# Kernel tuning notes

Hardware: AMD Instinct MI355X
Metric: run time of the kernel (lower is better)

Reference implementation:

```python
import jax, jax.numpy as jnp
import numpy as np

H, N_PATCH, F, DIM = 12, 196, 8, 768
DH = DIM // H            # 64
D3 = 3 * DH              # per-head dim after 3*dim projection = 192
SCALE = float(np.sqrt(DH) * H)
B, S = 8, 1 + N_PATCH * F  # 1569


def setup_inputs() -> dict:
    key = jax.random.key(0)
    ks = jax.random.split(key, 12)
    w = lambda k, shp: (jax.random.normal(k, shp, dtype=jnp.float32) * 0.02)
    return {
        "x": jax.random.normal(ks[0], (B, S, DIM), dtype=jnp.float32),
        "Wq": w(ks[1], (DIM, 3 * DIM)), "bq": jnp.zeros((3 * DIM,), jnp.float32),
        "Wk": w(ks[2], (DIM, 3 * DIM)), "bk": jnp.zeros((3 * DIM,), jnp.float32),
        "Wv": w(ks[3], (DIM, 3 * DIM)), "bv": jnp.zeros((3 * DIM,), jnp.float32),
        "Wt": w(ks[4], (3 * DIM, DIM)), "bt": jnp.zeros((DIM,), jnp.float32),
        "Wf": w(ks[5], (3 * DIM, DIM)), "bf": jnp.zeros((DIM,), jnp.float32),
    }


def _heads(t):
    # [b, s, 3*dim] -> [b, H, s, D3]
    b, s, _ = t.shape
    return t.reshape(b, s, H, D3).transpose(0, 2, 1, 3)


def _merge(t):
    # [b, H, s, D3] -> [b, s, 3*dim]
    b, _, s, _ = t.shape
    return t.transpose(0, 2, 1, 3).reshape(b, s, H * D3)


def _attn(q, k, v):
    a = jax.nn.softmax(jnp.einsum('bhqd,bhkd->bhqk', q, k) / SCALE, axis=-1)
    return jnp.einsum('bhqk,bhkd->bhqd', a, v)


def reference(x, Wq, bq, Wk, bk, Wv, bv, Wt, bt, Wf, bf):
    patches = x[:, 1:, :]                       # [b, n*F, dim]
    # NOTE: faithful to original code: v_mat comes from self.k, k_mat from self.v
    qm = _heads(patches @ Wq + bq)
    vm = _heads(patches @ Wk + bk)
    km = _heads(patches @ Wv + bv)

    # CLS attention over full sequence (here v from self.v, k from self.k)
    q_cls = _heads(x[:, 0:1, :] @ Wq + bq)      # [b,H,1,D3]
    v_cls = _heads(x @ Wv + bv)
    k_cls = _heads(x @ Wk + bk)
    inter_cls = _attn(q_cls, k_cls, v_cls)      # [b,H,1,D3]

    # Stage 1: temporal attention per patch (patches 1..n-1), vectorized.
    # tokens are frame-major: index = frame*n + patch, so slice p::n == patch p across frames
    def per_patch(t):
        b = t.shape[0]
        return t.reshape(b, H, F, N_PATCH, D3)[:, :, :, 1:, :].transpose(0, 1, 3, 2, 4)  # [b,H,n-1,F,D3]
    q5, k5, v5 = per_patch(qm), per_patch(km), per_patch(vm)
    a1 = jax.nn.softmax(jnp.einsum('bhpfd,bhpgd->bhpfg', q5, k5) / SCALE, axis=-1)
    t1 = jnp.einsum('bhpfg,bhpgd->bhpfd', a1, v5).sum(axis=3)   # [b,H,n-1,D3]
    t1 = jnp.tile(t1, (1, 1, F, 1))                              # [b,H,(n-1)*F,D3]
    ti = _merge(t1) @ Wt + bt                                    # [b,(n-1)*F,dim]

    # Stage 2 (same qkv swap as stage 1)
    q2 = _heads(ti @ Wq + bq)
    v2 = _heads(ti @ Wk + bk)
    k2 = _heads(ti @ Wv + bv)
    outs = [_attn(q2[:, :, 0:N_PATCH], k2[:, :, 0:N_PATCH], v2[:, :, 0:N_PATCH]).sum(axis=2, keepdims=True)]
    for xi in range(1, F):  # small fixed loop over num_frames
        o = _attn(q2[:, :, xi:xi + N_PATCH], k2[:, :, xi::N_PATCH], v2[:, :, xi::N_PATCH])
        outs.append(o.sum(axis=2, keepdims=True))
    t2 = jnp.concatenate(outs, axis=2)                           # [b,H,F,D3]
    t2 = jnp.tile(t2, (1, 1, N_PATCH, 1))                        # [b,H,F*n,D3]

    full = jnp.concatenate([inter_cls, t2], axis=2)              # [b,H,1+n*F,D3]
    return _merge(full) @ Wf + bf                                # [b,S,dim]
```

## Files before the change

### kernel.cpp

```cpp
#include <hip/hip_runtime.h>
#include <math.h>

#define B_    8
#define SEQ   1569
#define DIMX  768
#define H_    12
#define D3    192
#define F_    8
#define NP    196
#define P1    195
#define NCOL  2304
#define NS    6912
#define RSCALE (1.0f/96.0f)
#define NCHUNK 16
#define CH     99
#define CLS_STRIDE 196
#define PG4   49

typedef __bf16 bf16_t;
typedef bf16_t bf16x8 __attribute__((ext_vector_type(8)));
typedef float  f32x4  __attribute__((ext_vector_type(4)));

__device__ __forceinline__ void load_lds16(const bf16_t* g, bf16_t* l) {
  __builtin_amdgcn_global_load_lds(
      (const __attribute__((address_space(1))) void*)g,
      (__attribute__((address_space(3))) void*)l, 16, 0, 0);
}

__device__ __forceinline__ float block_max256(float v, float* red) {
  #pragma unroll
  for (int o = 32; o > 0; o >>= 1) v = fmaxf(v, __shfl_xor(v, o, 64));
  __syncthreads();
  if ((threadIdx.x & 63) == 0) red[threadIdx.x >> 6] = v;
  __syncthreads();
  return fmaxf(fmaxf(red[0], red[1]), fmaxf(red[2], red[3]));
}

__device__ __forceinline__ float block_sum256(float v, float* red) {
  #pragma unroll
  for (int o = 32; o > 0; o >>= 1) v += __shfl_xor(v, o, 64);
  __syncthreads();
  if ((threadIdx.x & 63) == 0) red[threadIdx.x >> 6] = v;
  __syncthreads();
  return red[0] + red[1] + red[2] + red[3];
}

__global__ __launch_bounds__(256) void cast_f32_bf16(
    const float* __restrict__ in, bf16_t* __restrict__ out, int n4) {
  const int i = blockIdx.x * 256 + threadIdx.x;
  if (i >= n4) return;
  const float4 v = ((const float4*)in)[i];
  bf16_t o4[4] = {(bf16_t)v.x, (bf16_t)v.y, (bf16_t)v.z, (bf16_t)v.w};
  ((uint2*)out)[i] = *(uint2*)o4;
}

__global__ __launch_bounds__(256) void concat_bias_kernel(
    const float* __restrict__ bq, const float* __restrict__ bk,
    const float* __restrict__ bv, float* __restrict__ qkvb) {
  const int i = blockIdx.x * 256 + threadIdx.x;
  if (i >= NS) return;
  float v;
  if (i < NCOL) v = bq[i];
  else if (i < 2 * NCOL) v = bk[i - NCOL];
  else v = bv[i - 2 * NCOL];
  qkvb[i] = v;
}

__global__ __launch_bounds__(256) void transpose_all(
    const float* __restrict__ Wq, const float* __restrict__ Wk,
    const float* __restrict__ Wv, const float* __restrict__ Wt,
    const float* __restrict__ Wf, bf16_t* __restrict__ WqkvT,
    bf16_t* __restrict__ WtT, bf16_t* __restrict__ WfT) {
  __shared__ float t[32][33];
  const int bid = blockIdx.x;
  const int mat = bid / 1728, tt = bid % 1728;
  const float* W; bf16_t* WT; int Kd, Nd, nt, kt;
  if (mat < 3) {
    Kd = DIMX; Nd = NCOL;
    W = (mat == 0) ? Wq : ((mat == 1) ? Wk : Wv);
    WT = WqkvT + (size_t)mat * NCOL * DIMX;
    nt = tt % 72; kt = tt / 72;
  } else {
    Kd = NCOL; Nd = DIMX;
    W = (mat == 3) ? Wt : Wf;
    WT = (mat == 3) ? WtT : WfT;
    nt = tt % 24; kt = tt / 24;
  }
  const int bn = nt * 32, bk = kt * 32;
  const int tx = threadIdx.x & 31, ty = threadIdx.x >> 5;
  #pragma unroll
  for (int i = 0; i < 32; i += 8)
    t[ty + i][tx] = W[(size_t)(bk + ty + i) * Nd + bn + tx];
  __syncthreads();
  #pragma unroll
  for (int i = 0; i < 32; i += 8)
    WT[(size_t)(bn + ty + i) * Kd + bk + tx] = (bf16_t)t[tx][ty + i];
}

__global__ __launch_bounds__(256) void gemm_mfma_bt(
    const bf16_t* __restrict__ A, const bf16_t* __restrict__ BT,
    const float* __restrict__ bias, void* __restrict__ C,
    int M, int N, int K, int MT, int NT, int GROUPM, int XCDB, int outBf16) {
  __shared__ bf16_t As[128 * 64];
  __shared__ bf16_t Bs[128 * 64];
  const int tid  = threadIdx.x;
  const int wave = tid >> 6, lane = tid & 63;

  int m_tile, n_tile;
  const int pid = blockIdx.x;
  if (XCDB > 0) {
    const int xcd = pid & 7, q = pid >> 3;
    m_tile = xcd * XCDB + q % XCDB;
    n_tile = q / XCDB;
    if (m_tile >= MT) return;
  } else {
    const int npg   = GROUPM * NT;
    const int group = pid / npg;
    const int first_m = group * GROUPM;
    int gsm = MT - first_m; if (gsm > GROUPM) gsm = GROUPM;
    const int lpid  = pid % npg;
    m_tile = first_m + lpid % gsm;
    n_tile = lpid / gsm;
  }
  const int row0 = m_tile * 128, col0 = n_tile * 128;

  const int fr = lane & 15, kg = lane >> 4;
  int ra0 = row0 + wave * 32 + fr;
  int ra1 = ra0 + 16;
  if (ra0 >= M) ra0 = M - 1;
  if (ra1 >= M) ra1 = M - 1;
  const bf16_t* Ap0 = A + (size_t)ra0 * K + kg * 8;
  const bf16_t* Ap1 = A + (size_t)ra1 * K + kg * 8;
  const bf16_t* Bp0 = BT + (size_t)(col0 + wave * 32 + fr) * K + kg * 8;
  const bf16_t* Bp1 = Bp0 + (size_t)16 * K;
  const int la0 = (wave * 2 + 0) * 1024, la1 = (wave * 2 + 1) * 1024;

  const int mb = (wave & 1) * 4,  nb = (wave >> 1) * 4;
  const int m0 = (wave & 1) * 64, n0 = (wave >> 1) * 64;
  f32x4 acc[4][4] = {};

  for (int k0 = 0; k0 < K; k0 += 64) {
    load_lds16(Ap0 + k0,      &As[la0]);
    load_lds16(Ap0 + k0 + 32, &As[la0 + 512]);
    load_lds16(Ap1 + k0,      &As[la1]);
    load_lds16(Ap1 + k0 + 32, &As[la1 + 512]);
    load_lds16(Bp0 + k0,      &Bs[la0]);
    load_lds16(Bp0 + k0 + 32, &Bs[la0 + 512]);
    load_lds16(Bp1 + k0,      &Bs[la1]);
    load_lds16(Bp1 + k0 + 32, &Bs[la1 + 512]);
    __syncthreads();

    #pragma unroll
    for (int h = 0; h < 2; ++h) {
      bf16x8 af[4], bfr[4];
      #pragma unroll
      for (int i = 0; i < 4; ++i) {
        af[i]  = *(const bf16x8*)&As[(mb + i) * 1024 + h * 512 + lane * 8];
        bfr[i] = *(const bf16x8*)&Bs[(nb + i) * 1024 + h * 512 + lane * 8];
      }
      #pragma unroll
      for (int i = 0; i < 4; ++i)
        #pragma unroll
        for (int j = 0; j < 4; ++j)
          acc[i][j] = __builtin_amdgcn_mfma_f32_16x16x32_bf16(
              af[i], bfr[j], acc[i][j], 0, 0, 0);
    }
    __syncthreads();
  }

  const int cc = lane & 15, cr4 = (lane >> 4) * 4;
  #pragma unroll
  for (int i = 0; i < 4; ++i) {
    #pragma unroll
    for (int j = 0; j < 4; ++j) {
      const int col = col0 + n0 + j * 16 + cc;
      const float bcol = bias[col];
      #pragma unroll
      for (int reg = 0; reg < 4; ++reg) {
        const int r = row0 + m0 + i * 16 + cr4 + reg;
        if (r < M) {
          const float v = acc[i][j][reg] + bcol;
          if (outBf16) ((bf16_t*)C)[(size_t)r * N + col] = (bf16_t)v;
          else         ((float*)C)[(size_t)r * N + col] = v;
        }
      }
    }
  }
}

__global__ __launch_bounds__(256) void xi0_scores_mfma(
    const bf16_t* __restrict__ QKV2, float* __restrict__ Smat) {
  __shared__ bf16_t As[128 * 32];
  __shared__ bf16_t Bs[128 * 32];
  const int tid  = threadIdx.x;
  const int wave = tid >> 6, lane = tid & 63;
  const int row0 = blockIdx.x * 128, col0 = blockIdx.y * 128;
  const int bh = blockIdx.z;
  const int b = bh / H_, h = bh % H_;
  const bf16_t* Abase = QKV2 + (size_t)b * P1 * NS + h * D3;
  const bf16_t* Bbase = QKV2 + (size_t)b * P1 * NS + 2 * NCOL + h * D3;

  const int fr = lane & 15, kg = lane >> 4;
  int ra0 = row0 + wave * 32 + fr;
  int ra1 = ra0 + 16;
  if (ra0 >= P1) ra0 = P1 - 1;
  if (ra1 >= P1) ra1 = P1 - 1;
  int cb0 = col0 + wave * 32 + fr;
  int cb1 = cb0 + 16;
  if (cb0 >= P1) cb0 = P1 - 1;
  if (cb1 >= P1) cb1 = P1 - 1;
  const bf16_t* Ap0 = Abase + (size_t)ra0 * NS + kg * 8;
  const bf16_t* Ap1 = Abase + (size_t)ra1 * NS + kg * 8;
  const bf16_t* Bp0 = Bbase + (size_t)cb0 * NS + kg * 8;
  const bf16_t* Bp1 = Bbase + (size_t)cb1 * NS + kg * 8;
  bf16_t* lA0 = &As[(wave * 2 + 0) * 512];
  bf16_t* lA1 = &As[(wave * 2 + 1) * 512];
  bf16_t* lB0 = &Bs[(wave * 2 + 0) * 512];
  bf16_t* lB1 = &Bs[(wave * 2 + 1) * 512];

  const int m0 = (wave & 1) * 64, n0 = (wave >> 1) * 64;
  const int mb = (wave & 1) * 4,  nb = (wave >> 1) * 4;
  f32x4 acc[4][4] = {};

  for (int k0 = 0; k0 < D3; k0 += 32) {
    load_lds16(Ap0 + k0, lA0);
    load_lds16(Ap1 + k0, lA1);
    load_lds16(Bp0 + k0, lB0);
    load_lds16(Bp1 + k0, lB1);
    __syncthreads();
    bf16x8 af[4], bfr[4];
    #pragma unroll
    for (int i = 0; i < 4; ++i) {
      af[i]  = *(const bf16x8*)&As[(mb + i) * 512 + lane * 8];
      bfr[i] = *(const bf16x8*)&Bs[(nb + i) * 512 + lane * 8];
    }
    #pragma unroll
    for (int i = 0; i < 4; ++i)
      #pragma unroll
      for (int j = 0; j < 4; ++j)
        acc[i][j] = __builtin_amdgcn_mfma_f32_16x16x32_bf16(
            af[i], bfr[j], acc[i][j], 0, 0, 0);
    __syncthreads();
  }

  float* S = Smat + (size_t)bh * P1 * P1;
  const int cc = lane & 15, cr4 = (lane >> 4) * 4;
  #pragma unroll
  for (int i = 0; i < 4; ++i)
    #pragma unroll
    for (int j = 0; j < 4; ++j) {
      const int col = col0 + n0 + j * 16 + cc;
      #pragma unroll
      for (int reg = 0; reg < 4; ++reg) {
        const int r = row0 + m0 + i * 16 + cr4 + reg;
        if (r < P1 && col < P1) S[(size_t)r * P1 + col] = acc[i][j][reg] * RSCALE;
      }
    }
}

__global__ __launch_bounds__(256) void xi0_finish_kernel(
    const float* __restrict__ Smat, const bf16_t* __restrict__ QKV2,
    bf16_t* __restrict__ FULL9b) {
  const int bh = blockIdx.x;
  const int b = bh / H_, h = bh % H_;
  __shared__ float mrow[P1], inv_l[P1], g[P1];
  const float* S = Smat + (size_t)bh * P1 * P1;
  const int tid = threadIdx.x;
  const int wave = tid >> 6, lane = tid & 63;

  for (int r = wave; r < P1; r += 4) {
    const float* Sr = S + (size_t)r * P1;
    const float s0 = Sr[lane];
    const float s1 = Sr[64 + lane];
    const float s2 = Sr[128 + lane];
    const float s3 = (lane < 3) ? Sr[192 + lane] : -1e30f;
    float m = fmaxf(fmaxf(s0, s1), fmaxf(s2, s3));
    #pragma unroll
    for (int o = 1; o < 64; o <<= 1) m = fmaxf(m, __shfl_xor(m, o, 64));
    float e = expf(s0 - m) * ((lane == 0) ? 2.f : 1.f) + expf(s1 - m) +
              expf(s2 - m) + ((lane < 3) ? expf(s3 - m) : 0.f);
    #pragma unroll
    for (int o = 1; o < 64; o <<= 1) e += __shfl_xor(e, o, 64);
    if (lane == 0) {
      mrow[r] = m;
      inv_l[r] = ((r == 0) ? 2.f : 1.f) / e;
    }
  }
  __syncthreads();
  if (tid < P1) {
    float s = 0.f;
    for (int r = 0; r < P1; ++r)
      s += expf(S[(size_t)r * P1 + tid] - mrow[r]) * inv_l[r];
    g[tid] = s * ((tid == 0) ? 2.f : 1.f);
  }
  __syncthreads();
  if (tid < D3) {
    float acc = 0.f;
    const bf16_t* vbase = QKV2 + (size_t)b * P1 * NS + NCOL + h * D3 + tid;
    for (int k = 0; k < P1; ++k)
      acc = fmaf(g[k], (float)vbase[(size_t)k * NS], acc);
    FULL9b[((size_t)b * 9 + 1) * NCOL + h * D3 + tid] = (bf16_t)acc;
  }
}

__global__ __launch_bounds__(256) void cls_part_kernel(
    const bf16_t* __restrict__ XQKV, float* __restrict__ CLSP, int b0) {
  const int h  = blockIdx.x % H_;
  const int bl = blockIdx.x / H_;
  const int b  = b0 + bl;
  const int c  = blockIdx.y;
  const int t0 = c * CH;
  const int tend = (t0 + CH < SEQ) ? t0 + CH : SEQ;
  __shared__ float qs[D3];
  __shared__ float sc[CH];
  __shared__ float red[4];
  const int tid = threadIdx.x;

  const bf16_t* Qr = XQKV + (size_t)bl * SEQ * NS + h * D3;
  if (tid < 24) {
    const bf16x8 q8 = *(const bf16x8*)(Qr + tid * 8);
    #pragma unroll
    for (int m2 = 0; m2 < 8; ++m2) qs[tid * 8 + m2] = (float)q8[m2];
  }
  __syncthreads();

  float lmax = -1e30f;
  for (int t = t0 + tid; t < tend; t += 256) {
    const bf16_t* kr = XQKV + ((size_t)bl * SEQ + t) * NS + NCOL + h * D3;
    float acc = 0.f;
    #pragma unroll 3
    for (int d = 0; d < D3; d += 8) {
      const bf16x8 k8 = *(const bf16x8*)(kr + d);
      #pragma unroll
      for (int m2 = 0; m2 < 8; ++m2) acc = fmaf(qs[d + m2], (float)k8[m2], acc);
    }
    acc *= RSCALE;
    sc[t - t0] = acc;
    lmax = fmaxf(lmax, acc);
  }
  const float m = block_max256(lmax, red);
  float lsum = 0.f;
  for (int t = t0 + tid; t < tend; t += 256) {
    const float e = expf(sc[t - t0] - m);
    sc[t - t0] = e;
    lsum += e;
  }
  const float L = block_sum256(lsum, red);
  __syncthreads();

  float* P = CLSP + ((size_t)(b * H_ + h) * NCHUNK + c) * CLS_STRIDE;
  if (tid < D3) {
    float acc = 0.f;
    const bf16_t* vbase = XQKV + ((size_t)bl * SEQ + t0) * NS + 2 * NCOL + h * D3 + tid;
    for (int t = t0; t < tend; ++t)
      acc = fmaf(sc[t - t0], (float)vbase[(size_t)(t - t0) * NS], acc);
    P[tid] = acc;
  }
  if (tid == 192) P[192] = m;
  if (tid == 193) P[193] = L;
}

__global__ __launch_bounds__(256) void cls_combine_kernel(
    const float* __restrict__ CLSP, bf16_t* __restrict__ FULL9b) {
  const int bh = blockIdx.x;
  const int tid = threadIdx.x;
  const float* P = CLSP + (size_t)bh * NCHUNK * CLS_STRIDE;

  float M = -1e30f;
  #pragma unroll
  for (int c = 0; c < NCHUNK; ++c) M = fmaxf(M, P[c * CLS_STRIDE + 192]);
  float L = 0.f;
  float w[NCHUNK];
  #pragma unroll
  for (int c = 0; c < NCHUNK; ++c) {
    w[c] = expf(P[c * CLS_STRIDE + 192] - M);
    L += P[c * CLS_STRIDE + 193] * w[c];
  }
  if (tid < D3) {
    float acc = 0.f;
    #pragma unroll
    for (int c = 0; c < NCHUNK; ++c)
      acc = fmaf(w[c], P[c * CLS_STRIDE + tid], acc);
    const int b = bh / H_, h = bh % H_;
    FULL9b[((size_t)b * 9 + 0) * NCOL + h * D3 + tid] = (bf16_t)(acc / L);
  }
}

__global__ __launch_bounds__(256) void temporal_kernel(
    const bf16_t* __restrict__ XQKV, bf16_t* __restrict__ T1U, int b0) {
  const int id = blockIdx.x;
  const int pg = id % PG4;
  const int h  = (id / PG4) % H_;
  const int bl = id / (PG4 * H_);
  const int b  = b0 + bl;
  const int wave = threadIdx.x >> 6, lane = threadIdx.x & 63;
  __shared__ float qs[4][8][196], ks[4][8][196];

  int pi = pg * 4 + wave;
  const bool act = (pi < P1);
  if (!act) pi = P1 - 1;

  #pragma unroll
  for (int i = 0; i < 6; ++i) {
    const int idx = lane + 64 * i;
    const int arr = idx / 192;
    const int c = idx % 192;
    const int f = c / 24, d0 = (c % 24) * 8;
    const size_t base = ((size_t)bl * SEQ + (size_t)f * NP + pi + 2) * NS +
                        (arr ? 2 * NCOL : 0) + h * D3 + d0;
    const bf16x8 v8 = *(const bf16x8*)(XQKV + base);
    float* dst = arr ? &ks[wave][f][d0] : &qs[wave][f][d0];
    #pragma unroll
    for (int m2 = 0; m2 < 8; ++m2) dst[m2] = (float)v8[m2];
  }
  __syncthreads();

  const int f = lane >> 3, g = lane & 7;
  float s = 0.f;
  for (int d = 0; d < D3; d += 4) {
    const float4 a4 = *(const float4*)&qs[wave][f][d];
    const float4 b4 = *(const float4*)&ks[wave][g][d];
    s = fmaf(a4.x, b4.x, s); s = fmaf(a4.y, b4.y, s);
    s = fmaf(a4.z, b4.z, s); s = fmaf(a4.w, b4.w, s);
  }
  s *= RSCALE;

  float m = s;
  #pragma unroll
  for (int o = 1; o < 8; o <<= 1) m = fmaxf(m, __shfl_xor(m, o, 64));
  const float e = expf(s - m);
  float sum = e;
  #pragma unroll
  for (int o = 1; o < 8; o <<= 1) sum += __shfl_xor(sum, o, 64);
  float a = e / sum;
  #pragma unroll
  for (int o = 8; o < 64; o <<= 1) a += __shfl_xor(a, o, 64);
  float wg[8];
  #pragma unroll
  for (int gg = 0; gg < 8; ++gg) wg[gg] = __shfl(a, gg, 64);

  if (act) {
    const size_t vrow = (size_t)bl * SEQ * NS + NCOL + h * D3;
    #pragma unroll
    for (int i = 0; i < 3; ++i) {
      const int d = lane + 64 * i;
      float o = 0.f;
      #pragma unroll
      for (int gg = 0; gg < 8; ++gg) {
        const bf16_t vv = XQKV[vrow + ((size_t)gg * NP + pi + 2) * NS + d];
        o = fmaf(wg[gg], (float)vv, o);
      }
      T1U[((size_t)b * P1 + pi) * NCOL + h * D3 + d] = (bf16_t)o;
    }
  }
}

__global__ __launch_bounds__(256) void stage2_xi_kernel(
    const bf16_t* __restrict__ QKV2, bf16_t* __restrict__ FULL9b) {
  const int xi = 1 + blockIdx.x % 7;
  const int h  = (blockIdx.x / 7) % H_;
  const int b  = blockIdx.x / (7 * H_);
  __shared__ float Ks[8][196], Vs[8][196], Qs[32][196];
  __shared__ float Pp[32][8];
  const int tid = threadIdx.x;

  for (int idx = tid; idx < 192; idx += 256) {
    const int k = idx / 24, d0 = (idx % 24) * 8;
    const bf16x8 v8 = *(const bf16x8*)(QKV2 + ((size_t)(b * P1 + xi + k)) * NS +
                                       2 * NCOL + h * D3 + d0);
    #pragma unroll
    for (int m2 = 0; m2 < 8; ++m2) Ks[k][d0 + m2] = (float)v8[m2];
  }
  for (int idx = tid; idx < 192; idx += 256) {
    const int k = idx / 24, d0 = (idx % 24) * 8;
    const bf16x8 v8 = *(const bf16x8*)(QKV2 + ((size_t)(b * P1 + xi + k)) * NS +
                                       NCOL + h * D3 + d0);
    #pragma unroll
    for (int m2 = 0; m2 < 8; ++m2) Vs[k][d0 + m2] = (float)v8[m2];
  }

  float acc = 0.f;
  for (int c = 0; c < 7; ++c) {
    __syncthreads();
    for (int idx = tid; idx < 768; idx += 256) {
      const int qr = idx / 24, d0 = (idx % 24) * 8;
      const int rq = c * 32 + qr;
      if (rq < P1) {
        const bf16x8 v8 = *(const bf16x8*)(QKV2 + ((size_t)(b * P1 + rq)) * NS +
                                           h * D3 + d0);
        #pragma unroll
        for (int m2 = 0; m2 < 8; ++m2) Qs[qr][d0 + m2] = (float)v8[m2];
      } else {
        #pragma unroll
        for (int m2 = 0; m2 < 8; ++m2) Qs[qr][d0 + m2] = 0.f;
      }
    }
    __syncthreads();
    const int grp = tid >> 3, k = tid & 7;
    float dot = 0.f;
    for (int d = 0; d < D3; d += 4) {
      const float4 a4 = *(const float4*)&Qs[grp][d];
      const float4 b4 = *(const float4*)&Ks[k][d];
      dot = fmaf(a4.x, b4.x, dot); dot = fmaf(a4.y, b4.y, dot);
      dot = fmaf(a4.z, b4.z, dot); dot = fmaf(a4.w, b4.w, dot);
    }
    dot *= RSCALE;
    float m = dot;
    #pragma unroll
    for (int o = 1; o < 8; o <<= 1) m = fmaxf(m, __shfl_xor(m, o, 64));
    const float e = expf(dot - m);
    float s = e;
    #pragma unroll
    for (int o = 1; o < 8; o <<= 1) s += __shfl_xor(s, o, 64);
    Pp[grp][k] = e / s;
    __syncthreads();
    if (tid < D3) {
      #pragma unroll 4
      for (int g2 = 0; g2 < 32; ++g2) {
        const int rq2 = c * 32 + g2;
        if (rq2 < P1) {
          const float mult = (rq2 == xi) ? 2.f : 1.f;
          float o = 0.f;
          #pragma unroll
          for (int kk = 0; kk < 8; ++kk) o = fmaf(Pp[g2][kk], Vs[kk][tid], o);
          acc = fmaf(mult, o, acc);
        }
      }
    }
  }
  if (tid < D3)
    FULL9b[((size_t)b * 9 + 1 + xi) * NCOL + h * D3 + tid] = (bf16_t)acc;
}

__global__ __launch_bounds__(256) void bcast_kernel(
    const float* __restrict__ OUT9, float* __restrict__ out) {
  const int idx = blockIdx.x * 256 + threadIdx.x;
  const int total = B_ * SEQ * (DIMX / 4);
  if (idx >= total) return;
  const int d4 = idx % (DIMX / 4);
  const int bs = idx / (DIMX / 4);
  const int s = bs % SEQ;
  const int b = bs / SEQ;
  const int row = (s == 0) ? 0 : 1 + ((s - 1) & 7);
  ((float4*)out)[idx] = ((const float4*)OUT9)[(size_t)(b * 9 + row) * (DIMX / 4) + d4];
}

extern "C" void kernel_launch(void* const* d_in, const int* in_sizes, int n_in,
                              void* d_out, int out_size, void* d_ws, size_t ws_size,
                              hipStream_t stream) {
  const float* x  = (const float*)d_in[0];
  const float* Wq = (const float*)d_in[1];
  const float* bq = (const float*)d_in[2];
  const float* Wk = (const float*)d_in[3];
  const float* bk = (const float*)d_in[4];
  const float* Wv = (const float*)d_in[5];
  const float* bv = (const float*)d_in[6];
  const float* Wt = (const float*)d_in[7];
  const float* bt = (const float*)d_in[8];
  const float* Wf = (const float*)d_in[9];
  const float* bf = (const float*)d_in[10];
  float* out = (float*)d_out;
  (void)in_sizes; (void)n_in; (void)out_size;

  char* ws = (char*)d_ws;
  size_t off = 0;
  auto alloc_f32 = [&](size_t elems) {
    size_t a = (off + 63) & ~(size_t)63;
    off = a + elems * sizeof(float);
    return (float*)(ws + a);
  };
  auto alloc_bf16 = [&](size_t elems) {
    size_t a = (off + 63) & ~(size_t)63;
    off = a + elems * sizeof(bf16_t);
    return (bf16_t*)(ws + a);
  };

  bf16_t* T1Ub   = alloc_bf16((size_t)B_ * P1 * NCOL);
  bf16_t* TIUb   = alloc_bf16((size_t)B_ * P1 * DIMX);
  bf16_t* QKV2b  = alloc_bf16((size_t)B_ * P1 * NS);
  bf16_t* FULL9b = alloc_bf16((size_t)B_ * 9 * NCOL);
  float*  OUT9   = alloc_f32((size_t)B_ * 9 * DIMX);
  float*  Smat   = alloc_f32((size_t)B_ * H_ * P1 * P1);
  float*  CLSP   = alloc_f32((size_t)B_ * H_ * NCHUNK * CLS_STRIDE);
  float*  QKVbias= alloc_f32(NS);
  bf16_t* WqkvT  = alloc_bf16((size_t)3 * NCOL * DIMX);
  bf16_t* WtT    = alloc_bf16((size_t)DIMX * NCOL);
  bf16_t* WfT    = alloc_bf16((size_t)DIMX * NCOL);

  const size_t remain = (ws_size > off) ? (ws_size - off) : 0;
  int Bc = 8;
  while (Bc > 1 &&
         (size_t)Bc * SEQ * (NS + DIMX) * sizeof(bf16_t) + 512 > remain)
    Bc >>= 1;
  bf16_t* XQKVb = alloc_bf16((size_t)Bc * SEQ * NS);
  bf16_t* xb    = alloc_bf16((size_t)Bc * SEQ * DIMX);

  transpose_all<<<dim3(1728 * 5), 256, 0, stream>>>(
      Wq, Wk, Wv, Wt, Wf, WqkvT, WtT, WfT);
  concat_bias_kernel<<<dim3((NS + 255) / 256), 256, 0, stream>>>(bq, bk, bv, QKVbias);

  for (int b0 = 0; b0 < B_; b0 += Bc) {
    const int Mrows = Bc * SEQ;
    const int n4 = Mrows * DIMX / 4;
    cast_f32_bf16<<<dim3((n4 + 255) / 256), 256, 0, stream>>>(
        x + (size_t)b0 * SEQ * DIMX, xb, n4);
    const int MT = (Mrows + 127) / 128, NT = NS / 128;
    const int XCDB = (MT + 7) / 8;
    gemm_mfma_bt<<<dim3(8 * XCDB * NT), 256, 0, stream>>>(
        xb, WqkvT, QKVbias, XQKVb, Mrows, NS, DIMX, MT, NT, 0, XCDB, 1);
    cls_part_kernel<<<dim3(Bc * H_, NCHUNK), 256, 0, stream>>>(XQKVb, CLSP, b0);
    temporal_kernel<<<dim3(Bc * H_ * PG4), 256, 0, stream>>>(XQKVb, T1Ub, b0);
  }
  cls_combine_kernel<<<dim3(B_ * H_), 256, 0, stream>>>(CLSP, FULL9b);

  {
    const int MT = (B_ * P1 + 127) / 128, NT = DIMX / 128;
    gemm_mfma_bt<<<dim3(MT * NT), 256, 0, stream>>>(
        T1Ub, WtT, bt, TIUb, B_ * P1, DIMX, NCOL, MT, NT, 4, 0, 1);
  }
  {
    const int MT = (B_ * P1 + 127) / 128, NT = NS / 128;
    gemm_mfma_bt<<<dim3(MT * NT), 256, 0, stream>>>(
        TIUb, WqkvT, QKVbias, QKV2b, B_ * P1, NS, DIMX, MT, NT, 4, 0, 1);
  }

  xi0_scores_mfma<<<dim3(2, 2, B_ * H_), 256, 0, stream>>>(QKV2b, Smat);
  xi0_finish_kernel<<<dim3(B_ * H_), 256, 0, stream>>>(Smat, QKV2b, FULL9b);
  stage2_xi_kernel<<<dim3(B_ * H_ * 7), 256, 0, stream>>>(QKV2b, FULL9b);

  {
    const int MT = 1, NT = DIMX / 128;
    gemm_mfma_bt<<<dim3(MT * NT), 256, 0, stream>>>(
        FULL9b, WfT, bf, OUT9, B_ * 9, DIMX, NCOL, MT, NT, 1, 0, 0);
  }

  {
    const int total4 = B_ * SEQ * (DIMX / 4);
    bcast_kernel<<<dim3((total4 + 255) / 256), 256, 0, stream>>>(OUT9, out);
  }
}
```

Baseline: 816.4 us.

## Pre-swizzle weights and input into MFMA fragment panels for contiguous LDS loads

Transposed weights and the bf16-cast input are now written in a tiled panel layout of 16 rows by 32 k per 512-element block, matching the MFMA fragment order. The GEMM then loads each wave's LDS tile from one contiguous 1KB span instead of strided rows. This targets global-load coalescing in the QKV projection and the other weight-side loads. It also drops the XCD-aware tile mapping in favour of grouped-M ordering and pads the input buffer to a multiple of 128 rows.

```diff
diff --git a/kernel.cpp b/kernel.cpp
--- a/kernel.cpp
+++ b/kernel.cpp
@@ -45,15 +45,6 @@
   return red[0] + red[1] + red[2] + red[3];
 }
 
-__global__ __launch_bounds__(256) void cast_f32_bf16(
-    const float* __restrict__ in, bf16_t* __restrict__ out, int n4) {
-  const int i = blockIdx.x * 256 + threadIdx.x;
-  if (i >= n4) return;
-  const float4 v = ((const float4*)in)[i];
-  bf16_t o4[4] = {(bf16_t)v.x, (bf16_t)v.y, (bf16_t)v.z, (bf16_t)v.w};
-  ((uint2*)out)[i] = *(uint2*)o4;
-}
-
 __global__ __launch_bounds__(256) void concat_bias_kernel(
     const float* __restrict__ bq, const float* __restrict__ bk,
     const float* __restrict__ bv, float* __restrict__ qkvb) {
@@ -64,6 +55,25 @@
   else if (i < 2 * NCOL) v = bk[i - NCOL];
   else v = bv[i - 2 * NCOL];
   qkvb[i] = v;
+}
+
+__global__ __launch_bounds__(256) void cast_swizzle(
+    const float* __restrict__ x, bf16_t* __restrict__ out, int Mreal) {
+  const int ms = blockIdx.x;
+  const int wave = threadIdx.x >> 6, lane = threadIdx.x & 63;
+  const int KP = DIMX / 32;
+  int row = ms * 16 + (lane & 15);
+  if (row >= Mreal) row = Mreal - 1;
+  const int cb = (lane >> 4) * 8;
+  const float* src = x + (size_t)row * DIMX + cb;
+  bf16_t* dst = out + ((size_t)ms * KP) * 512 + lane * 8;
+  for (int kp = wave; kp < KP; kp += 4) {
+    const float4 a = *(const float4*)(src + kp * 32);
+    const float4 b = *(const float4*)(src + kp * 32 + 4);
+    bf16_t o8[8] = {(bf16_t)a.x, (bf16_t)a.y, (bf16_t)a.z, (bf16_t)a.w,
+                    (bf16_t)b.x, (bf16_t)b.y, (bf16_t)b.z, (bf16_t)b.w};
+    *(uint4*)(dst + (size_t)kp * 512) = *(uint4*)o8;
+  }
 }
 
 __global__ __launch_bounds__(256) void transpose_all(
@@ -87,43 +97,44 @@
     nt = tt % 24; kt = tt / 24;
   }
   const int bn = nt * 32, bk = kt * 32;
+  const int KP = Kd >> 5;
   const int tx = threadIdx.x & 31, ty = threadIdx.x >> 5;
   #pragma unroll
   for (int i = 0; i < 32; i += 8)
     t[ty + i][tx] = W[(size_t)(bk + ty + i) * Nd + bn + tx];
   __syncthreads();
-  #pragma unroll
-  for (int i = 0; i < 32; i += 8)
-    WT[(size_t)(bn + ty + i) * Kd + bk + tx] = (bf16_t)t[tx][ty + i];
+  const int k = bk + tx;
+  #pragma unroll
+  for (int i = 0; i < 32; i += 8) {
+    const int n = bn + ty + i;
+    const size_t off = ((size_t)(n >> 4) * KP + (k >> 5)) * 512 +
+                       ((n & 15) + 16 * ((k >> 3) & 3)) * 8 + (k & 7);
+    WT[off] = (bf16_t)t[tx][ty + i];
+  }
 }
 
 __global__ __launch_bounds__(256) void gemm_mfma_bt(
     const bf16_t* __restrict__ A, const bf16_t* __restrict__ BT,
     const float* __restrict__ bias, void* __restrict__ C,
-    int M, int N, int K, int MT, int NT, int GROUPM, int XCDB, int outBf16) {
+    int M, int N, int K, int MT, int NT, int GROUPM, int aSwz, int outBf16) {
   __shared__ bf16_t As[128 * 64];
   __shared__ bf16_t Bs[128 * 64];
   const int tid  = threadIdx.x;
   const int wave = tid >> 6, lane = tid & 63;
 
-  int m_tile, n_tile;
-  const int pid = blockIdx.x;
-  if (XCDB > 0) {
-    const int xcd = pid & 7, q = pid >> 3;
-    m_tile = xcd * XCDB + q % XCDB;
-    n_tile = q / XCDB;
-    if (m_tile >= MT) return;
-  } else {
-    const int npg   = GROUPM * NT;
-    const int group = pid / npg;
-    const int first_m = group * GROUPM;
-    int gsm = MT - first_m; if (gsm > GROUPM) gsm = GROUPM;
-    const int lpid  = pid % npg;
-    m_tile = first_m + lpid % gsm;
-    n_tile = lpid / gsm;
-  }
+  const int pid   = blockIdx.x;
+  const int npg   = GROUPM * NT;
+  const int group = pid / npg;
+  const int first_m = group * GROUPM;
+  int gsm = MT - first_m; if (gsm > GROUPM) gsm = GROUPM;
+  const int lpid  = pid % npg;
+  const int m_tile = first_m + lpid % gsm;
+  const int n_tile = lpid / gsm;
   const int row0 = m_tile * 128, col0 = n_tile * 128;
 
+  const int KP = K >> 5;
+  const bf16_t* Bpan = BT + ((size_t)(n_tile * 8 + wave * 2) * KP) * 512 + lane * 8;
+  const bf16_t* Apan = A + ((size_t)(m_tile * 8 + wave * 2) * KP) * 512 + lane * 8;
   const int fr = lane & 15, kg = lane >> 4;
   int ra0 = row0 + wave * 32 + fr;
   int ra1 = ra0 + 16;
@@ -131,23 +142,29 @@
   if (ra1 >= M) ra1 = M - 1;
   const bf16_t* Ap0 = A + (size_t)ra0 * K + kg * 8;
   const bf16_t* Ap1 = A + (size_t)ra1 * K + kg * 8;
-  const bf16_t* Bp0 = BT + (size_t)(col0 + wave * 32 + fr) * K + kg * 8;
-  const bf16_t* Bp1 = Bp0 + (size_t)16 * K;
+
   const int la0 = (wave * 2 + 0) * 1024, la1 = (wave * 2 + 1) * 1024;
-
   const int mb = (wave & 1) * 4,  nb = (wave >> 1) * 4;
   const int m0 = (wave & 1) * 64, n0 = (wave >> 1) * 64;
   f32x4 acc[4][4] = {};
 
-  for (int k0 = 0; k0 < K; k0 += 64) {
-    load_lds16(Ap0 + k0,      &As[la0]);
-    load_lds16(Ap0 + k0 + 32, &As[la0 + 512]);
-    load_lds16(Ap1 + k0,      &As[la1]);
-    load_lds16(Ap1 + k0 + 32, &As[la1 + 512]);
-    load_lds16(Bp0 + k0,      &Bs[la0]);
-    load_lds16(Bp0 + k0 + 32, &Bs[la0 + 512]);
-    load_lds16(Bp1 + k0,      &Bs[la1]);
-    load_lds16(Bp1 + k0 + 32, &Bs[la1 + 512]);
+  for (int kk = 0; kk < K; kk += 64) {
+    const int kp = kk >> 5;
+    if (aSwz) {
+      load_lds16(Apan + (size_t)kp * 512,            &As[la0]);
+      load_lds16(Apan + (size_t)(kp + 1) * 512,      &As[la0 + 512]);
+      load_lds16(Apan + (size_t)(KP + kp) * 512,     &As[la1]);
+      load_lds16(Apan + (size_t)(KP + kp + 1) * 512, &As[la1 + 512]);
+    } else {
+      load_lds16(Ap0 + kk,      &As[la0]);
+      load_lds16(Ap0 + kk + 32, &As[la0 + 512]);
+      load_lds16(Ap1 + kk,      &As[la1]);
+      load_lds16(Ap1 + kk + 32, &As[la1 + 512]);
+    }
+    load_lds16(Bpan + (size_t)kp * 512,            &Bs[la0]);
+    load_lds16(Bpan + (size_t)(kp + 1) * 512,      &Bs[la0 + 512]);
+    load_lds16(Bpan + (size_t)(KP + kp) * 512,     &Bs[la1]);
+    load_lds16(Bpan + (size_t)(KP + kp + 1) * 512, &Bs[la1 + 512]);
     __syncthreads();
 
     #pragma unroll
@@ -590,10 +607,11 @@
   const size_t remain = (ws_size > off) ? (ws_size - off) : 0;
   int Bc = 8;
   while (Bc > 1 &&
-         (size_t)Bc * SEQ * (NS + DIMX) * sizeof(bf16_t) + 512 > remain)
+         (size_t)(Bc * SEQ + 128) * (NS + DIMX) * sizeof(bf16_t) + 512 > remain)
     Bc >>= 1;
+  const int MTmax = (Bc * SEQ + 127) / 128;
   bf16_t* XQKVb = alloc_bf16((size_t)Bc * SEQ * NS);
-  bf16_t* xb    = alloc_bf16((size_t)Bc * SEQ * DIMX);
+  bf16_t* xb    = alloc_bf16((size_t)MTmax * 128 * DIMX);
 
   transpose_all<<<dim3(1728 * 5), 256, 0, stream>>>(
       Wq, Wk, Wv, Wt, Wf, WqkvT, WtT, WfT);
@@ -601,13 +619,11 @@
 
   for (int b0 = 0; b0 < B_; b0 += Bc) {
     const int Mrows = Bc * SEQ;
-    const int n4 = Mrows * DIMX / 4;
-    cast_f32_bf16<<<dim3((n4 + 255) / 256), 256, 0, stream>>>(
-        x + (size_t)b0 * SEQ * DIMX, xb, n4);
     const int MT = (Mrows + 127) / 128, NT = NS / 128;
-    const int XCDB = (MT + 7) / 8;
-    gemm_mfma_bt<<<dim3(8 * XCDB * NT), 256, 0, stream>>>(
-        xb, WqkvT, QKVbias, XQKVb, Mrows, NS, DIMX, MT, NT, 0, XCDB, 1);
+    cast_swizzle<<<dim3(MT * 8), 256, 0, stream>>>(
+        x + (size_t)b0 * SEQ * DIMX, xb, Mrows);
+    gemm_mfma_bt<<<dim3(MT * NT), 256, 0, stream>>>(
+        xb, WqkvT, QKVbias, XQKVb, Mrows, NS, DIMX, MT, NT, 8, 1, 1);
     cls_part_kernel<<<dim3(Bc * H_, NCHUNK), 256, 0, stream>>>(XQKVb, CLSP, b0);
     temporal_kernel<<<dim3(Bc * H_ * PG4), 256, 0, stream>>>(XQKVb, T1Ub, b0);
   }
```

Measured after the change: 669.2 us. -18.0%, faster.
